# Kernel optimization log

Hardware: AMD Instinct MI355X
Metric: run time of the kernel (lower is better)

Reference implementation:

```python
import jax, jax.numpy as jnp
import numpy as np

TAU = 2.0        # tau_m
EPS = 1e-5       # BatchNorm eps
SG_GAIN = 4.0    # surrogate gradient gain for LIF nodes
GATE_GAIN = 10.0 # SCALPerceptionLayer gain
GATE_VTH = 0.5   # SCALPerceptionLayer v_th_init


def _spike(v, v_th, gain):
    # Heaviside forward, sigmoid surrogate backward (straight-through).
    s = jax.nn.sigmoid(gain * (v - v_th))
    hard = (v >= v_th).astype(v.dtype)
    return s + jax.lax.stop_gradient(hard - s)


def _lif(x, v_th):
    # single-step LIF, zero initial membrane: v = v0 + (x - v0)/tau = x/tau
    return _spike(x / TAU, v_th, SG_GAIN)


def _bn(x, gamma, beta):
    # BatchNorm1d over channel dim D of (B, N, D): stats over (B, N)
    m = x.mean(axis=(0, 1))
    v = x.var(axis=(0, 1))
    return (x - m) * jax.lax.rsqrt(v + EPS) * gamma + beta


def setup_inputs() -> dict:
    B, N, D, H = 4, 1024, 1024, 16
    key = jax.random.key(0)
    ks = jax.random.split(key, 12)
    def lin(k, out_f, in_f):
        return jax.random.normal(k, (out_f, in_f), jnp.float32) * (in_f ** -0.5)
    inp = {"x": jax.random.normal(ks[0], (B, N, D), jnp.float32)}
    for i, nm in enumerate(["q", "k", "v", "p"]):
        inp[f"W{nm}"] = lin(ks[1 + i], D, D)
        inp[f"b{nm}"] = jnp.zeros((D,), jnp.float32)
        inp[f"g{nm}"] = jnp.ones((D,), jnp.float32)   # BN gamma
        inp[f"beta{nm}"] = jnp.zeros((D,), jnp.float32)  # BN beta
    inp["Wg"] = lin(ks[10], H, D)  # logic_core linear
    inp["bg"] = jnp.zeros((H,), jnp.float32)
    return inp


def reference(x, Wq, bq, gq, betaq, Wk, bk, gk, betak,
              Wv, bv, gv, betav, Wp, bp, gp, betap, Wg, bg):
    B, N, D = x.shape
    H = Wg.shape[0]
    hd = D // H
    scale = hd ** -0.125

    def branch(W, b, g, beta):
        # Linear -> BN (over channels) -> LIF spike -> (B,H,N,hd)
        s = _lif(_bn(x @ W.T + b, g, beta), 1.0)
        return s.reshape(B, N, H, hd).transpose(0, 2, 1, 3)

    q = branch(Wq, bq, gq, betaq)
    k = branch(Wk, bk, gk, betak)
    v = branch(Wv, bv, gv, betav)

    # LogicGateController: energy (B,H) -> repeat to (B,D) -> spiking linear gate
    energy = (q * k).sum(axis=-1).mean(axis=-1)            # (B, H)
    energy_feat = jnp.tile(energy, (1, D // H))            # (B, D)
    gate = _spike(energy_feat @ Wg.T + bg, GATE_VTH, GATE_GAIN)  # (B, H)
    gate = gate[:, :, None, None]                          # (B, H, 1, 1)

    attn = jnp.einsum('bhnd,bhmd->bhnm', q, k) * scale     # (B,H,N,N)
    x_attn = jnp.einsum('bhnm,bhmd->bhnd', attn * gate, v) # (B,H,N,hd)
    x_attn = x_attn.transpose(0, 2, 1, 3).reshape(B, N, D)
    x_attn = _lif(x_attn, 0.5)                             # attn_lif, v_th=0.5

    out = _lif(_bn(x_attn @ Wp.T + bp, gp, betap), 1.0)    # proj path
    return out
```

## Files before the change

### kernel.cpp

```cpp
#include <hip/hip_runtime.h>
#include <cstddef>
#include <cstdint>

#define EPS 1e-5f

typedef __bf16 bf16x8 __attribute__((ext_vector_type(8)));
typedef float f32x4 __attribute__((ext_vector_type(4)));
typedef unsigned short u16x8 __attribute__((ext_vector_type(8)));

__device__ __forceinline__ unsigned short f2bf(float f) {
  unsigned u = __builtin_bit_cast(unsigned, f);
  unsigned r = u + 0x7FFFu + ((u >> 16) & 1u);
  return (unsigned short)(r >> 16);
}
__device__ __forceinline__ float bf2f(unsigned short h) {
  unsigned u = (unsigned)h << 16;
  return __builtin_bit_cast(float, u);
}

__device__ __forceinline__ void gl_lds16(const void* g, void* l) {
  __builtin_amdgcn_global_load_lds(
      (const __attribute__((address_space(1))) unsigned int*)g,
      (__attribute__((address_space(3))) unsigned int*)l, 16, 0, 0);
}

template <int MODE>
__global__ __launch_bounds__(512) void gemm8_bf16_bt(
    const unsigned short* __restrict__ A,
    const unsigned short* __restrict__ W0, const unsigned short* __restrict__ W1,
    const float* __restrict__ b0, const float* __restrict__ b1,
    unsigned short* __restrict__ Y, double* __restrict__ psum, double* __restrict__ psq,
    const int* __restrict__ flags, int N, int Kc)
{
  if (MODE == 2) { if (flags[0] == 0) return; }

  __shared__ unsigned short As[2][8192];
  __shared__ unsigned short Bs[2][8192];
  const int tid = threadIdx.x;

  const int bid = blockIdx.x + (blockIdx.y << 3) + (blockIdx.z << 8);
  const int nwg = (int)gridDim.z << 8;
  const int cpx = nwg >> 3;
  const int sw = (bid & 7) * cpx + (bid >> 3);
  const int bx = sw & 7, by = (sw >> 3) & 31, z = sw >> 8;

  if (MODE == 1) { if (flags[1 + (by >> 3)] == 0) return; }

  const unsigned short* Bm = z ? W1 : W0;
  const float* bias = z ? b1 : b0;
  unsigned short* Yz = Y + (size_t)z * 4096 * N;

  const int bm = by * 128, bn = bx * 128;
  const int lane = tid & 63, w = tid >> 6;
  const int wr = w >> 2, wc = w & 3;
  const int l15 = lane & 15, g = lane >> 4;

  f32x4 acc[4][2] = {};

  const unsigned short* aSrc[2]; const unsigned short* bSrc[2]; int dOff[2];
#pragma unroll
  for (int c = 0; c < 2; ++c) {
    int S = c * 512 + tid;
    int row = S >> 3, sp = S & 7;
    int sl = sp ^ (row & 7);
    aSrc[c] = A  + (size_t)(bm + row) * Kc + sl * 8;
    bSrc[c] = Bm + (size_t)(bn + row) * Kc + sl * 8;
    dOff[c] = S * 8;
  }
  int aOff[4][2], bOff[2][2];
#pragma unroll
  for (int t = 0; t < 2; ++t) {
#pragma unroll
    for (int i = 0; i < 4; ++i) {
      int rowA = wr * 64 + i * 16 + l15;
      aOff[i][t] = rowA * 64 + ((t * 4 + g) ^ (rowA & 7)) * 8;
    }
#pragma unroll
    for (int j = 0; j < 2; ++j) {
      int rowB = wc * 32 + j * 16 + l15;
      bOff[j][t] = rowB * 64 + ((t * 4 + g) ^ (rowB & 7)) * 8;
    }
  }

  const int nk = Kc >> 6;
#pragma unroll
  for (int c = 0; c < 2; ++c) { gl_lds16(aSrc[c], &As[0][dOff[c]]); aSrc[c] += 64; }
#pragma unroll
  for (int c = 0; c < 2; ++c) { gl_lds16(bSrc[c], &Bs[0][dOff[c]]); bSrc[c] += 64; }

  int cur = 0;
  for (int kt = 0; kt < nk; ++kt) {
    if (kt + 1 < nk) {
#pragma unroll
      for (int c = 0; c < 2; ++c) { gl_lds16(aSrc[c], &As[cur ^ 1][dOff[c]]); aSrc[c] += 64; }
#pragma unroll
      for (int c = 0; c < 2; ++c) { gl_lds16(bSrc[c], &Bs[cur ^ 1][dOff[c]]); bSrc[c] += 64; }
      asm volatile("s_waitcnt vmcnt(4)" ::: "memory");
    } else {
      asm volatile("s_waitcnt vmcnt(0)" ::: "memory");
    }
    __builtin_amdgcn_s_barrier();
    __builtin_amdgcn_sched_barrier(0);
    {
      const unsigned short* Ac = &As[cur][0];
      const unsigned short* Bc = &Bs[cur][0];
#pragma unroll
      for (int t = 0; t < 2; ++t) {
        bf16x8 af[4], bfr[2];
#pragma unroll
        for (int i = 0; i < 4; ++i) af[i] = *(const bf16x8*)&Ac[aOff[i][t]];
#pragma unroll
        for (int j = 0; j < 2; ++j) bfr[j] = *(const bf16x8*)&Bc[bOff[j][t]];
#pragma unroll
        for (int i = 0; i < 4; ++i)
#pragma unroll
          for (int j = 0; j < 2; ++j)
            acc[i][j] = __builtin_amdgcn_mfma_f32_16x16x32_bf16(af[i], bfr[j], acc[i][j], 0, 0, 0);
      }
    }
    __builtin_amdgcn_s_barrier();
    cur ^= 1;
  }

  const int r0 = bm + wr * 64 + g * 4;
  float csum[2], csq[2];
#pragma unroll
  for (int j = 0; j < 2; ++j) { csum[j] = 0.f; csq[j] = 0.f; }
#pragma unroll
  for (int j = 0; j < 2; ++j) {
    int col = bn + wc * 32 + j * 16 + l15;
    float bv = bias[col];
#pragma unroll
    for (int i = 0; i < 4; ++i)
#pragma unroll
      for (int r = 0; r < 4; ++r) {
        float yv = acc[i][j][r] + bv;
        unsigned short h = f2bf(yv);
        float yb = bf2f(h);
        Yz[(size_t)(r0 + i * 16 + r) * N + col] = h;
        csum[j] += yb;
        csq[j] += yb * yb;
      }
  }
  __syncthreads();
  float* Ls = (float*)&As[0][0];
  const int slot = wr * 4 + g;
#pragma unroll
  for (int j = 0; j < 2; ++j) {
    int ci = wc * 32 + j * 16 + l15;
    Ls[slot * 128 + ci] = csum[j];
    Ls[1024 + slot * 128 + ci] = csq[j];
  }
  __syncthreads();
  if (tid < 128) {
    double s = 0.0, q = 0.0;
#pragma unroll
    for (int sl = 0; sl < 8; ++sl) {
      s += (double)Ls[sl * 128 + tid];
      q += (double)Ls[1024 + sl * 128 + tid];
    }
    size_t o = ((size_t)z * 32 + by) * N + bn + tid;
    psum[o] = s;
    psq[o] = q;
  }
}

__global__ void prep1_kernel(const float* __restrict__ x,
                             const float* __restrict__ Wq, const float* __restrict__ Wk,
                             unsigned short* __restrict__ Xh, unsigned short* __restrict__ Wh3)
{
  int bid = blockIdx.x, tid = threadIdx.x;
  const float* src; unsigned short* dst; size_t base;
  if (bid < 2048) {
    src = x; dst = Xh; base = ((size_t)bid * 256 + tid) * 8;
  } else if (bid < 2560) {
    src = Wq; dst = Wh3; base = ((size_t)(bid - 2048) * 256 + tid) * 8;
  } else {
    src = Wk; dst = Wh3 + (size_t)1024 * 1024; base = ((size_t)(bid - 2560) * 256 + tid) * 8;
  }
  float4 a = *reinterpret_cast<const float4*>(&src[base]);
  float4 b = *reinterpret_cast<const float4*>(&src[base + 4]);
  u16x8 o;
  o[0] = f2bf(a.x); o[1] = f2bf(a.y); o[2] = f2bf(a.z); o[3] = f2bf(a.w);
  o[4] = f2bf(b.x); o[5] = f2bf(b.y); o[6] = f2bf(b.z); o[7] = f2bf(b.w);
  *reinterpret_cast<u16x8*>(&dst[base]) = o;
}

__global__ void prep2_kernel(const float* __restrict__ Wv, const float* __restrict__ Wp,
                             unsigned short* __restrict__ Whv, unsigned short* __restrict__ Wpcat,
                             const int* __restrict__ flags)
{
  if (flags[0] == 0) return;
  int bid = blockIdx.x, tid = threadIdx.x;
  if (bid < 512) {
    size_t base = ((size_t)bid * 256 + tid) * 8;
    float4 a = *reinterpret_cast<const float4*>(&Wv[base]);
    float4 b = *reinterpret_cast<const float4*>(&Wv[base + 4]);
    u16x8 o;
    o[0] = f2bf(a.x); o[1] = f2bf(a.y); o[2] = f2bf(a.z); o[3] = f2bf(a.w);
    o[4] = f2bf(b.x); o[5] = f2bf(b.y); o[6] = f2bf(b.z); o[7] = f2bf(b.w);
    *reinterpret_cast<u16x8*>(&Whv[base]) = o;
  } else {
    size_t base = ((size_t)(bid - 512) * 256 + tid) * 8;
    int r = (int)(base >> 10), c = (int)(base & 1023);
    float4 a = *reinterpret_cast<const float4*>(&Wp[base]);
    float4 b = *reinterpret_cast<const float4*>(&Wp[base + 4]);
    u16x8 hi, lo;
    hi[0] = f2bf(a.x); lo[0] = f2bf(a.x - bf2f(hi[0]));
    hi[1] = f2bf(a.y); lo[1] = f2bf(a.y - bf2f(hi[1]));
    hi[2] = f2bf(a.z); lo[2] = f2bf(a.z - bf2f(hi[2]));
    hi[3] = f2bf(a.w); lo[3] = f2bf(a.w - bf2f(hi[3]));
    hi[4] = f2bf(b.x); lo[4] = f2bf(b.x - bf2f(hi[4]));
    hi[5] = f2bf(b.y); lo[5] = f2bf(b.y - bf2f(hi[5]));
    hi[6] = f2bf(b.z); lo[6] = f2bf(b.z - bf2f(hi[6]));
    hi[7] = f2bf(b.w); lo[7] = f2bf(b.w - bf2f(hi[7]));
    unsigned short* Or = Wpcat + (size_t)r * 2048;
    *reinterpret_cast<u16x8*>(&Or[c]) = hi;
    *reinterpret_cast<u16x8*>(&Or[1024 + c]) = lo;
  }
}

__global__ void bn_finalize(const double* __restrict__ psum, const double* __restrict__ psq,
                            const float* __restrict__ g0, const float* __restrict__ g1,
                            float* __restrict__ meanv, float* __restrict__ Av,
                            const int* __restrict__ runflag,
                            int* __restrict__ zflags, int* __restrict__ zenergy,
                            int N, double invM)
{
  if (zflags && blockIdx.x == 0 && blockIdx.y == 0) {
    int t = threadIdx.x;
    if (t < 5) zflags[t] = 0;
    if (t >= 64 && t < 128) zenergy[t - 64] = 0;
  }
  if (runflag && runflag[0] == 0) return;
  int z = blockIdx.y;
  const float* g = z ? g1 : g0;
  int c = blockIdx.x * blockDim.x + threadIdx.x;
  const double* ps = psum + (size_t)z * 32 * N + c;
  const double* pq = psq  + (size_t)z * 32 * N + c;
  double s0 = 0, s1 = 0, q0 = 0, q1 = 0;
#pragma unroll
  for (int rb = 0; rb < 32; rb += 2) {
    s0 += ps[(size_t)rb * N];       q0 += pq[(size_t)rb * N];
    s1 += ps[(size_t)(rb + 1) * N]; q1 += pq[(size_t)(rb + 1) * N];
  }
  double s = s0 + s1, q = q0 + q1;
  double m = s * invM;
  double var = q * invM - m * m;
  if (var < 0.0) var = 0.0;
  meanv[(size_t)z * N + c] = (float)m;
  Av[(size_t)z * N + c] = g[(size_t)c] * rsqrtf((float)var + EPS);
}

__global__ void bn_finalize_p(const double* __restrict__ psum, const double* __restrict__ psq,
                              const float* __restrict__ gp, const float* __restrict__ bp,
                              float* __restrict__ meanv, float* __restrict__ Av,
                              const int* __restrict__ flags, int N, double invM)
{
  int c = blockIdx.x * blockDim.x + threadIdx.x;
  float ybb = bf2f(f2bf(bp[c]));
  double yd = (double)ybb;
  double s = 0.0, q = 0.0;
  for (int rb = 0; rb < 32; ++rb) {
    if (flags[1 + (rb >> 3)]) {
      s += psum[(size_t)rb * N + c];
      q += psq [(size_t)rb * N + c];
    } else {
      s += 128.0 * yd;
      q += 128.0 * yd * yd;
    }
  }
  double m = s * invM;
  double var = q * invM - m * m;
  if (var < 0.0) var = 0.0;
  meanv[c] = (float)m;
  Av[c] = gp[(size_t)c] * rsqrtf((float)var + EPS);
}

__global__ void energy_cnt(const unsigned short* __restrict__ Yq,
                           const unsigned short* __restrict__ Yk,
                           const float* __restrict__ meanv, const float* __restrict__ Av,
                           const float* __restrict__ beq, const float* __restrict__ bek,
                           int* __restrict__ energy_int, int N)
{
  const int tid = threadIdx.x;
  const int c0 = (tid * 8) & (N - 1);
  const int head = c0 >> 6;
  const int batch = blockIdx.x >> 7;
  const float* mq = meanv;     const float* aq = Av;
  const float* mk = meanv + N; const float* ak = Av + N;
  __shared__ int bins[16];
  if (tid < 16) bins[tid] = 0;
  __syncthreads();
  int cnt = 0;
#pragma unroll
  for (int j = 0; j < 4; ++j) {
    size_t base = (size_t)blockIdx.x * 8192 + j * 2048 + tid * 8;
    u16x8 yq = *reinterpret_cast<const u16x8*>(&Yq[base]);
    u16x8 yk = *reinterpret_cast<const u16x8*>(&Yk[base]);
#pragma unroll
    for (int e = 0; e < 8; ++e) {
      bool sq = (bf2f(yq[e]) - mq[c0 + e]) * aq[c0 + e] + beq[c0 + e] >= 2.0f;
      bool sk = (bf2f(yk[e]) - mk[c0 + e]) * ak[c0 + e] + bek[c0 + e] >= 2.0f;
      cnt += (sq && sk) ? 1 : 0;
    }
  }
  atomicAdd(&bins[head], cnt);
  __syncthreads();
  if (tid < 16) atomicAdd(&energy_int[batch * 16 + tid], bins[tid]);
}

__global__ void spike_qk_write(const unsigned short* __restrict__ Yq,
                               const unsigned short* __restrict__ Yk,
                               const float* __restrict__ meanv, const float* __restrict__ Av,
                               const float* __restrict__ beq, const float* __restrict__ bek,
                               unsigned short* __restrict__ qb, unsigned short* __restrict__ kb,
                               const int* __restrict__ flags, int N)
{
  if (flags[0] == 0) return;
  size_t base = ((size_t)blockIdx.x * 256 + threadIdx.x) * 8;
  int c0 = (int)(base & (size_t)(N - 1));
  const float* mq = meanv;     const float* aq = Av;
  const float* mk = meanv + N; const float* ak = Av + N;
  u16x8 yq = *reinterpret_cast<const u16x8*>(&Yq[base]);
  u16x8 yk = *reinterpret_cast<const u16x8*>(&Yk[base]);
  u16x8 oq, ok;
#pragma unroll
  for (int e = 0; e < 8; ++e) {
    oq[e] = ((bf2f(yq[e]) - mq[c0 + e]) * aq[c0 + e] + beq[c0 + e] >= 2.0f) ? 0x3F80 : 0;
    ok[e] = ((bf2f(yk[e]) - mk[c0 + e]) * ak[c0 + e] + bek[c0 + e] >= 2.0f) ? 0x3F80 : 0;
  }
  *reinterpret_cast<u16x8*>(&qb[base]) = oq;
  *reinterpret_cast<u16x8*>(&kb[base]) = ok;
}

__global__ void spike_v(const unsigned short* __restrict__ Yv,
                        const float* __restrict__ meanv, const float* __restrict__ Av,
                        const float* __restrict__ beta, unsigned short* __restrict__ vb,
                        const int* __restrict__ flags, int N)
{
  if (flags[0] == 0) return;
  size_t base = ((size_t)blockIdx.x * 256 + threadIdx.x) * 8;
  int c0 = (int)(base & (size_t)(N - 1));
  u16x8 y8 = *reinterpret_cast<const u16x8*>(&Yv[base]);
  u16x8 o;
#pragma unroll
  for (int e = 0; e < 8; ++e)
    o[e] = ((bf2f(y8[e]) - meanv[c0 + e]) * Av[c0 + e] + beta[c0 + e] >= 2.0f) ? 0x3F80 : 0;
  *reinterpret_cast<u16x8*>(&vb[base]) = o;
}

__global__ void bn_spike_f32(const unsigned short* __restrict__ Y,
                             const float* __restrict__ meanv, const float* __restrict__ Av,
                             const float* __restrict__ beta, const float* __restrict__ bp,
                             const int* __restrict__ flags, float* __restrict__ S, int N)
{
  size_t base = ((size_t)blockIdx.x * 256 + threadIdx.x) * 8;
  int c0 = (int)(base & (size_t)(N - 1));
  int batch = (int)(base >> 20);
  float y[8];
  if (flags[1 + batch]) {
    u16x8 y8 = *reinterpret_cast<const u16x8*>(&Y[base]);
#pragma unroll
    for (int e = 0; e < 8; ++e) y[e] = bf2f(y8[e]);
  } else {
#pragma unroll
    for (int e = 0; e < 8; ++e) y[e] = bf2f(f2bf(bp[c0 + e]));
  }
  float4 o0, o1;
  o0.x = ((y[0] - meanv[c0 + 0]) * Av[c0 + 0] + beta[c0 + 0] >= 2.0f) ? 1.f : 0.f;
  o0.y = ((y[1] - meanv[c0 + 1]) * Av[c0 + 1] + beta[c0 + 1] >= 2.0f) ? 1.f : 0.f;
  o0.z = ((y[2] - meanv[c0 + 2]) * Av[c0 + 2] + beta[c0 + 2] >= 2.0f) ? 1.f : 0.f;
  o0.w = ((y[3] - meanv[c0 + 3]) * Av[c0 + 3] + beta[c0 + 3] >= 2.0f) ? 1.f : 0.f;
  o1.x = ((y[4] - meanv[c0 + 4]) * Av[c0 + 4] + beta[c0 + 4] >= 2.0f) ? 1.f : 0.f;
  o1.y = ((y[5] - meanv[c0 + 5]) * Av[c0 + 5] + beta[c0 + 5] >= 2.0f) ? 1.f : 0.f;
  o1.z = ((y[6] - meanv[c0 + 6]) * Av[c0 + 6] + beta[c0 + 6] >= 2.0f) ? 1.f : 0.f;
  o1.w = ((y[7] - meanv[c0 + 7]) * Av[c0 + 7] + beta[c0 + 7] >= 2.0f) ? 1.f : 0.f;
  *reinterpret_cast<float4*>(&S[base]) = o0;
  *reinterpret_cast<float4*>(&S[base + 4]) = o1;
}

__global__ void gate_kernel(const int* __restrict__ energy_int, const float* __restrict__ Wg,
                            const float* __restrict__ bg, float* __restrict__ gate,
                            int* __restrict__ flags, int D)
{
  int b = blockIdx.x >> 4, hp = blockIdx.x & 15;
  int tid = threadIdx.x;
  float e[16];
#pragma unroll
  for (int h = 0; h < 16; ++h) e[h] = (float)energy_int[b * 16 + h] * (1.f / 1024.f);
  float s = 0.f;
  for (int j = tid; j < D; j += 256) s = fmaf(e[j & 15], Wg[(size_t)hp * D + j], s);
  __shared__ float red[256];
  red[tid] = s;
  __syncthreads();
  for (int off = 128; off; off >>= 1) {
    if (tid < off) red[tid] += red[tid + off];
    __syncthreads();
  }
  if (tid == 0) {
    int gv = (red[0] + bg[hp] >= 0.5f) ? 1 : 0;
    gate[blockIdx.x] = (float)gv;
    if (gv) { atomicOr(&flags[0], 1); atomicOr(&flags[1 + b], 1); }
  }
}

__global__ __launch_bounds__(256) void attn_kernel(
    const unsigned short* __restrict__ qb, const unsigned short* __restrict__ kb,
    const unsigned short* __restrict__ vb, const float* __restrict__ gate,
    const int* __restrict__ flags, unsigned short* __restrict__ xs,
    int Ntok, int D, float scale)
{
  int bh = blockIdx.x;
  int b = bh >> 4, h = bh & 15;
  if (flags[1 + b] == 0) return;
  int n0 = blockIdx.y * 32;
  int tid = threadIdx.x;
  unsigned short* outbase = xs + (size_t)(b * Ntok + n0) * 2048 + h * 64;

  if (gate[bh] == 0.f) {
    ushort4 zv = {0, 0, 0, 0};
    for (int i = tid; i < 32 * 16; i += 256) {
      int r = i >> 4, c4 = (i & 15) << 2;
      *reinterpret_cast<ushort4*>(&outbase[(size_t)r * 2048 + c4]) = zv;
      *reinterpret_cast<ushort4*>(&outbase[(size_t)r * 2048 + 1024 + c4]) = zv;
    }
    return;
  }

  __shared__ float qs[32][68], ks[32][68], vs[32][68], Ss[32][36];
  const unsigned short* qg = qb + (size_t)b * Ntok * D + h * 64;
  const unsigned short* kg = kb + (size_t)b * Ntok * D + h * 64;
  const unsigned short* vg = vb + (size_t)b * Ntok * D + h * 64;

  {
    int r = tid >> 3, c8 = (tid & 7) * 8;
    u16x8 t = *reinterpret_cast<const u16x8*>(&qg[(size_t)(n0 + r) * D + c8]);
#pragma unroll
    for (int e = 0; e < 8; ++e) qs[r][c8 + e] = bf2f(t[e]);
  }

  float acc[8];
#pragma unroll
  for (int j = 0; j < 8; ++j) acc[j] = 0.f;
  const int nloc = tid >> 3;
  const int dd0 = (tid & 7) * 8;

  for (int mt = 0; mt < Ntok / 32; ++mt) {
    int m0 = mt * 32;
    __syncthreads();
    {
      int r = tid >> 3, c8 = (tid & 7) * 8;
      u16x8 tk = *reinterpret_cast<const u16x8*>(&kg[(size_t)(m0 + r) * D + c8]);
      u16x8 tv = *reinterpret_cast<const u16x8*>(&vg[(size_t)(m0 + r) * D + c8]);
#pragma unroll
      for (int e = 0; e < 8; ++e) { ks[r][c8 + e] = bf2f(tk[e]); vs[r][c8 + e] = bf2f(tv[e]); }
    }
    __syncthreads();
    {
      int np = tid >> 3;
      int mp0 = (tid & 7) * 4;
      float s0 = 0.f, s1 = 0.f, s2 = 0.f, s3 = 0.f;
#pragma unroll 8
      for (int d = 0; d < 64; ++d) {
        float qv = qs[np][d];
        s0 = fmaf(qv, ks[mp0 + 0][d], s0);
        s1 = fmaf(qv, ks[mp0 + 1][d], s1);
        s2 = fmaf(qv, ks[mp0 + 2][d], s2);
        s3 = fmaf(qv, ks[mp0 + 3][d], s3);
      }
      Ss[np][mp0 + 0] = s0; Ss[np][mp0 + 1] = s1;
      Ss[np][mp0 + 2] = s2; Ss[np][mp0 + 3] = s3;
    }
    __syncthreads();
#pragma unroll 8
    for (int mp = 0; mp < 32; ++mp) {
      float sv = Ss[nloc][mp];
#pragma unroll
      for (int j = 0; j < 8; ++j) acc[j] = fmaf(sv, vs[mp][dd0 + j], acc[j]);
    }
  }

#pragma unroll
  for (int j = 0; j < 8; ++j) {
    float x = scale * acc[j];
    unsigned short sp = (x >= 1.0f) ? 0x3F80 : 0;
    outbase[(size_t)nloc * 2048 + dd0 + j] = sp;
    outbase[(size_t)nloc * 2048 + 1024 + dd0 + j] = sp;
  }
}

extern "C" void kernel_launch(void* const* d_in, const int* in_sizes, int n_in,
                              void* d_out, int out_size, void* d_ws, size_t ws_size,
                              hipStream_t stream)
{
  (void)in_sizes; (void)n_in; (void)out_size; (void)ws_size;
  const int Ntok = 1024, D = 1024;
  const int M = 4096;
  const float scale = 0.5946035575013605f;

  const float* x     = (const float*)d_in[0];
  const float* Wq    = (const float*)d_in[1];
  const float* bq    = (const float*)d_in[2];
  const float* gq    = (const float*)d_in[3];
  const float* betaq = (const float*)d_in[4];
  const float* Wk    = (const float*)d_in[5];
  const float* bk    = (const float*)d_in[6];
  const float* gk    = (const float*)d_in[7];
  const float* betak = (const float*)d_in[8];
  const float* Wv    = (const float*)d_in[9];
  const float* bv    = (const float*)d_in[10];
  const float* gv    = (const float*)d_in[11];
  const float* betav = (const float*)d_in[12];
  const float* Wp    = (const float*)d_in[13];
  const float* bp    = (const float*)d_in[14];
  const float* gp    = (const float*)d_in[15];
  const float* betap = (const float*)d_in[16];
  const float* Wg    = (const float*)d_in[17];
  const float* bg    = (const float*)d_in[18];

  char* w = (char*)d_ws;
  const size_t MB = 1024 * 1024;
  const size_t MN = (size_t)M * D;
  unsigned short* Y3bf  = (unsigned short*)(w + 0 * MB);
  unsigned short* xat2  = (unsigned short*)(w + 0 * MB);
  unsigned short* Yv    = Y3bf + 2 * MN;
  unsigned short* Yp    = (unsigned short*)(w + 24 * MB);
  unsigned short* Wpcat = (unsigned short*)(w + 32 * MB);
  unsigned short* Xh    = (unsigned short*)(w + 48 * MB);
  unsigned short* Wh3   = (unsigned short*)(w + 56 * MB);
  unsigned short* qb2   = (unsigned short*)(w + 62 * MB);
  unsigned short* kb2   = (unsigned short*)(w + 70 * MB);
  unsigned short* vb2   = (unsigned short*)(w + 78 * MB);
  double* psum   = (double*)(w + 86 * MB);
  double* psq    = (double*)(w + 87 * MB);
  float*  meanv  = (float*)(w + 88 * MB);
  float*  Av     = (float*)(w + 88 * MB + 16384);
  int*    energy_int = (int*)(w + 88 * MB + 32768);
  int*    flags  = (int*)(w + 88 * MB + 32768 + 512);
  float*  gate   = (float*)(w + 88 * MB + 32768 + 1024);

  float* out = (float*)d_out;
  unsigned short* Whq = Wh3;
  unsigned short* Whk = Wh3 + MN / 4;
  unsigned short* Whv = Wh3 + MN / 2;
  float* meanp = meanv + 3 * D;
  float* Avp   = Av + 3 * D;

  prep1_kernel<<<dim3(3072), 256, 0, stream>>>(x, Wq, Wk, Xh, Wh3);

  gemm8_bf16_bt<0><<<dim3(8, 32, 2), 512, 0, stream>>>(
      Xh, Whq, Whk, bq, bk, Y3bf, psum, psq, nullptr, D, 1024);
  bn_finalize<<<dim3(4, 2), 256, 0, stream>>>(
      psum, psq, gq, gk, meanv, Av, nullptr, flags, energy_int, D, 1.0 / M);

  energy_cnt<<<dim3(512), 256, 0, stream>>>(
      Y3bf, Y3bf + MN, meanv, Av, betaq, betak, energy_int, D);
  gate_kernel<<<dim3(64), 256, 0, stream>>>(energy_int, Wg, bg, gate, flags, D);

  spike_qk_write<<<dim3(2048), 256, 0, stream>>>(
      Y3bf, Y3bf + MN, meanv, Av, betaq, betak, qb2, kb2, flags, D);
  prep2_kernel<<<dim3(1024), 256, 0, stream>>>(Wv, Wp, Whv, Wpcat, flags);
  gemm8_bf16_bt<2><<<dim3(8, 32, 1), 512, 0, stream>>>(
      Xh, Whv, Whv, bv, bv, Yv, psum + 2 * 32 * (size_t)D, psq + 2 * 32 * (size_t)D,
      flags, D, 1024);
  bn_finalize<<<dim3(4, 1), 256, 0, stream>>>(
      psum + 2 * 32 * (size_t)D, psq + 2 * 32 * (size_t)D, gv, gv,
      meanv + 2 * D, Av + 2 * D, flags, nullptr, nullptr, D, 1.0 / M);
  spike_v<<<dim3(2048), 256, 0, stream>>>(Yv, meanv + 2 * D, Av + 2 * D, betav, vb2, flags, D);

  attn_kernel<<<dim3(64, Ntok / 32), 256, 0, stream>>>(
      qb2, kb2, vb2, gate, flags, xat2, Ntok, D, scale);

  gemm8_bf16_bt<1><<<dim3(8, 32, 1), 512, 0, stream>>>(
      xat2, Wpcat, Wpcat, bp, bp, Yp, psum, psq, flags, D, 2048);
  bn_finalize_p<<<dim3(4), 256, 0, stream>>>(psum, psq, gp, bp, meanp, Avp, flags, D, 1.0 / M);
  bn_spike_f32<<<dim3(2048), 256, 0, stream>>>(Yp, meanp, Avp, betap, bp, flags, out, D);
}
```

Before: 84.79 us.

## Use 256-thread GEMM with 4x4 MFMA tiles per wave and fused QK output

```diff
diff --git a/kernel.cpp b/kernel.cpp
--- a/kernel.cpp
+++ b/kernel.cpp
@@ -24,10 +24,9 @@
       (__attribute__((address_space(3))) unsigned int*)l, 16, 0, 0);
 }
 
-template <int MODE>
-__global__ __launch_bounds__(512) void gemm8_bf16_bt(
-    const unsigned short* __restrict__ A,
-    const unsigned short* __restrict__ W0, const unsigned short* __restrict__ W1,
+template <int MODE, int NX>
+__global__ __launch_bounds__(256) void gemm4_bf16_bt(
+    const unsigned short* __restrict__ A, const unsigned short* __restrict__ Bmat,
     const float* __restrict__ b0, const float* __restrict__ b1,
     unsigned short* __restrict__ Y, double* __restrict__ psum, double* __restrict__ psq,
     const int* __restrict__ flags, int N, int Kc)
@@ -38,64 +37,56 @@
   __shared__ unsigned short Bs[2][8192];
   const int tid = threadIdx.x;
 
-  const int bid = blockIdx.x + (blockIdx.y << 3) + (blockIdx.z << 8);
-  const int nwg = (int)gridDim.z << 8;
-  const int cpx = nwg >> 3;
+  constexpr int NXL = (NX == 16) ? 4 : 3;
+  const int bid = blockIdx.x + (blockIdx.y << NXL);
+  const int cpx = (NX * 32) >> 3;
   const int sw = (bid & 7) * cpx + (bid >> 3);
-  const int bx = sw & 7, by = (sw >> 3) & 31, z = sw >> 8;
+  const int bx = sw & (NX - 1), by = sw >> NXL;
 
   if (MODE == 1) { if (flags[1 + (by >> 3)] == 0) return; }
-
-  const unsigned short* Bm = z ? W1 : W0;
-  const float* bias = z ? b1 : b0;
-  unsigned short* Yz = Y + (size_t)z * 4096 * N;
 
   const int bm = by * 128, bn = bx * 128;
   const int lane = tid & 63, w = tid >> 6;
-  const int wr = w >> 2, wc = w & 3;
+  const int wr = w >> 1, wc = w & 1;
   const int l15 = lane & 15, g = lane >> 4;
 
-  f32x4 acc[4][2] = {};
-
-  const unsigned short* aSrc[2]; const unsigned short* bSrc[2]; int dOff[2];
-#pragma unroll
-  for (int c = 0; c < 2; ++c) {
-    int S = c * 512 + tid;
+  f32x4 acc[4][4] = {};
+
+  const unsigned short* aSrc[4]; const unsigned short* bSrc[4]; int dOff[4];
+#pragma unroll
+  for (int c = 0; c < 4; ++c) {
+    int S = c * 256 + tid;
     int row = S >> 3, sp = S & 7;
     int sl = sp ^ (row & 7);
-    aSrc[c] = A  + (size_t)(bm + row) * Kc + sl * 8;
-    bSrc[c] = Bm + (size_t)(bn + row) * Kc + sl * 8;
+    aSrc[c] = A    + (size_t)(bm + row) * Kc + sl * 8;
+    bSrc[c] = Bmat + (size_t)(bn + row) * Kc + sl * 8;
     dOff[c] = S * 8;
   }
-  int aOff[4][2], bOff[2][2];
-#pragma unroll
-  for (int t = 0; t < 2; ++t) {
-#pragma unroll
-    for (int i = 0; i < 4; ++i) {
+  int aOff[4][2], bOff[4][2];
+#pragma unroll
+  for (int i = 0; i < 4; ++i)
+#pragma unroll
+    for (int t = 0; t < 2; ++t) {
       int rowA = wr * 64 + i * 16 + l15;
       aOff[i][t] = rowA * 64 + ((t * 4 + g) ^ (rowA & 7)) * 8;
-    }
-#pragma unroll
-    for (int j = 0; j < 2; ++j) {
-      int rowB = wc * 32 + j * 16 + l15;
-      bOff[j][t] = rowB * 64 + ((t * 4 + g) ^ (rowB & 7)) * 8;
-    }
-  }
+      int rowB = wc * 64 + i * 16 + l15;
+      bOff[i][t] = rowB * 64 + ((t * 4 + g) ^ (rowB & 7)) * 8;
+    }
 
   const int nk = Kc >> 6;
 #pragma unroll
-  for (int c = 0; c < 2; ++c) { gl_lds16(aSrc[c], &As[0][dOff[c]]); aSrc[c] += 64; }
-#pragma unroll
-  for (int c = 0; c < 2; ++c) { gl_lds16(bSrc[c], &Bs[0][dOff[c]]); bSrc[c] += 64; }
+  for (int c = 0; c < 4; ++c) { gl_lds16(aSrc[c], &As[0][dOff[c]]); aSrc[c] += 64; }
+#pragma unroll
+  for (int c = 0; c < 4; ++c) { gl_lds16(bSrc[c], &Bs[0][dOff[c]]); bSrc[c] += 64; }
 
   int cur = 0;
   for (int kt = 0; kt < nk; ++kt) {
     if (kt + 1 < nk) {
 #pragma unroll
-      for (int c = 0; c < 2; ++c) { gl_lds16(aSrc[c], &As[cur ^ 1][dOff[c]]); aSrc[c] += 64; }
-#pragma unroll
-      for (int c = 0; c < 2; ++c) { gl_lds16(bSrc[c], &Bs[cur ^ 1][dOff[c]]); bSrc[c] += 64; }
-      asm volatile("s_waitcnt vmcnt(4)" ::: "memory");
+      for (int c = 0; c < 4; ++c) { gl_lds16(aSrc[c], &As[cur ^ 1][dOff[c]]); aSrc[c] += 64; }
+#pragma unroll
+      for (int c = 0; c < 4; ++c) { gl_lds16(bSrc[c], &Bs[cur ^ 1][dOff[c]]); bSrc[c] += 64; }
+      asm volatile("s_waitcnt vmcnt(8)" ::: "memory");
     } else {
       asm volatile("s_waitcnt vmcnt(0)" ::: "memory");
     }
@@ -106,15 +97,15 @@
       const unsigned short* Bc = &Bs[cur][0];
 #pragma unroll
       for (int t = 0; t < 2; ++t) {
-        bf16x8 af[4], bfr[2];
+        bf16x8 af[4], bfr[4];
 #pragma unroll
         for (int i = 0; i < 4; ++i) af[i] = *(const bf16x8*)&Ac[aOff[i][t]];
 #pragma unroll
-        for (int j = 0; j < 2; ++j) bfr[j] = *(const bf16x8*)&Bc[bOff[j][t]];
+        for (int j = 0; j < 4; ++j) bfr[j] = *(const bf16x8*)&Bc[bOff[j][t]];
 #pragma unroll
         for (int i = 0; i < 4; ++i)
 #pragma unroll
-          for (int j = 0; j < 2; ++j)
+          for (int j = 0; j < 4; ++j)
             acc[i][j] = __builtin_amdgcn_mfma_f32_16x16x32_bf16(af[i], bfr[j], acc[i][j], 0, 0, 0);
       }
     }
@@ -123,13 +114,13 @@
   }
 
   const int r0 = bm + wr * 64 + g * 4;
-  float csum[2], csq[2];
-#pragma unroll
-  for (int j = 0; j < 2; ++j) { csum[j] = 0.f; csq[j] = 0.f; }
-#pragma unroll
-  for (int j = 0; j < 2; ++j) {
-    int col = bn + wc * 32 + j * 16 + l15;
-    float bv = bias[col];
+  float csum[4], csq[4];
+#pragma unroll
+  for (int j = 0; j < 4; ++j) { csum[j] = 0.f; csq[j] = 0.f; }
+#pragma unroll
+  for (int j = 0; j < 4; ++j) {
+    int col = bn + wc * 64 + j * 16 + l15;
+    float bv = (MODE == 0) ? ((col >> 10) ? b1[col & 1023] : b0[col]) : b0[col];
 #pragma unroll
     for (int i = 0; i < 4; ++i)
 #pragma unroll
@@ -137,7 +128,7 @@
         float yv = acc[i][j][r] + bv;
         unsigned short h = f2bf(yv);
         float yb = bf2f(h);
-        Yz[(size_t)(r0 + i * 16 + r) * N + col] = h;
+        Y[(size_t)(r0 + i * 16 + r) * N + col] = h;
         csum[j] += yb;
         csq[j] += yb * yb;
       }
@@ -146,8 +137,8 @@
   float* Ls = (float*)&As[0][0];
   const int slot = wr * 4 + g;
 #pragma unroll
-  for (int j = 0; j < 2; ++j) {
-    int ci = wc * 32 + j * 16 + l15;
+  for (int j = 0; j < 4; ++j) {
+    int ci = wc * 64 + j * 16 + l15;
     Ls[slot * 128 + ci] = csum[j];
     Ls[1024 + slot * 128 + ci] = csq[j];
   }
@@ -159,7 +150,7 @@
       s += (double)Ls[sl * 128 + tid];
       q += (double)Ls[1024 + sl * 128 + tid];
     }
-    size_t o = ((size_t)z * 32 + by) * N + bn + tid;
+    size_t o = (size_t)by * N + bn + tid;
     psum[o] = s;
     psq[o] = q;
   }
@@ -220,42 +211,62 @@
   }
 }
 
-__global__ void bn_finalize(const double* __restrict__ psum, const double* __restrict__ psq,
-                            const float* __restrict__ g0, const float* __restrict__ g1,
-                            float* __restrict__ meanv, float* __restrict__ Av,
-                            const int* __restrict__ runflag,
-                            int* __restrict__ zflags, int* __restrict__ zenergy,
-                            int N, double invM)
-{
-  if (zflags && blockIdx.x == 0 && blockIdx.y == 0) {
+__global__ void bn_finalize_qk(const double* __restrict__ psum, const double* __restrict__ psq,
+                               const float* __restrict__ gq, const float* __restrict__ gk,
+                               float* __restrict__ meanv, float* __restrict__ Av,
+                               int* __restrict__ zflags, int* __restrict__ zenergy,
+                               double invM)
+{
+  if (blockIdx.x == 0) {
     int t = threadIdx.x;
     if (t < 5) zflags[t] = 0;
     if (t >= 64 && t < 128) zenergy[t - 64] = 0;
   }
-  if (runflag && runflag[0] == 0) return;
-  int z = blockIdx.y;
-  const float* g = z ? g1 : g0;
   int c = blockIdx.x * blockDim.x + threadIdx.x;
-  const double* ps = psum + (size_t)z * 32 * N + c;
-  const double* pq = psq  + (size_t)z * 32 * N + c;
+  const double* ps = psum + c;
+  const double* pq = psq + c;
   double s0 = 0, s1 = 0, q0 = 0, q1 = 0;
 #pragma unroll
   for (int rb = 0; rb < 32; rb += 2) {
-    s0 += ps[(size_t)rb * N];       q0 += pq[(size_t)rb * N];
-    s1 += ps[(size_t)(rb + 1) * N]; q1 += pq[(size_t)(rb + 1) * N];
+    s0 += ps[(size_t)rb * 2048];       q0 += pq[(size_t)rb * 2048];
+    s1 += ps[(size_t)(rb + 1) * 2048]; q1 += pq[(size_t)(rb + 1) * 2048];
   }
   double s = s0 + s1, q = q0 + q1;
   double m = s * invM;
   double var = q * invM - m * m;
   if (var < 0.0) var = 0.0;
-  meanv[(size_t)z * N + c] = (float)m;
-  Av[(size_t)z * N + c] = g[(size_t)c] * rsqrtf((float)var + EPS);
+  float gv = (c >> 10) ? gk[c & 1023] : gq[c];
+  meanv[c] = (float)m;
+  Av[c] = gv * rsqrtf((float)var + EPS);
+}
+
+__global__ void bn_finalize_v(const double* __restrict__ psum, const double* __restrict__ psq,
+                              const float* __restrict__ gv,
+                              float* __restrict__ meanv, float* __restrict__ Av,
+                              const int* __restrict__ runflag, double invM)
+{
+  if (runflag[0] == 0) return;
+  int c = blockIdx.x * blockDim.x + threadIdx.x;
+  const double* ps = psum + c;
+  const double* pq = psq + c;
+  double s0 = 0, s1 = 0, q0 = 0, q1 = 0;
+#pragma unroll
+  for (int rb = 0; rb < 32; rb += 2) {
+    s0 += ps[(size_t)rb * 1024];       q0 += pq[(size_t)rb * 1024];
+    s1 += ps[(size_t)(rb + 1) * 1024]; q1 += pq[(size_t)(rb + 1) * 1024];
+  }
+  double s = s0 + s1, q = q0 + q1;
+  double m = s * invM;
+  double var = q * invM - m * m;
+  if (var < 0.0) var = 0.0;
+  meanv[c] = (float)m;
+  Av[c] = gv[(size_t)c] * rsqrtf((float)var + EPS);
 }
 
 __global__ void bn_finalize_p(const double* __restrict__ psum, const double* __restrict__ psq,
                               const float* __restrict__ gp, const float* __restrict__ bp,
                               float* __restrict__ meanv, float* __restrict__ Av,
-                              const int* __restrict__ flags, int N, double invM)
+                              const int* __restrict__ flags, double invM)
 {
   int c = blockIdx.x * blockDim.x + threadIdx.x;
   float ybb = bf2f(f2bf(bp[c]));
@@ -263,8 +274,8 @@
   double s = 0.0, q = 0.0;
   for (int rb = 0; rb < 32; ++rb) {
     if (flags[1 + (rb >> 3)]) {
-      s += psum[(size_t)rb * N + c];
-      q += psq [(size_t)rb * N + c];
+      s += psum[(size_t)rb * 1024 + c];
+      q += psq [(size_t)rb * 1024 + c];
     } else {
       s += 128.0 * yd;
       q += 128.0 * yd * yd;
@@ -277,27 +288,30 @@
   Av[c] = gp[(size_t)c] * rsqrtf((float)var + EPS);
 }
 
-__global__ void energy_cnt(const unsigned short* __restrict__ Yq,
-                           const unsigned short* __restrict__ Yk,
+__global__ void energy_cnt(const unsigned short* __restrict__ Yqk,
                            const float* __restrict__ meanv, const float* __restrict__ Av,
                            const float* __restrict__ beq, const float* __restrict__ bek,
-                           int* __restrict__ energy_int, int N)
+                           int* __restrict__ energy_int)
 {
   const int tid = threadIdx.x;
-  const int c0 = (tid * 8) & (N - 1);
+  const int half = tid >> 7;
+  const int tloc = tid & 127;
+  const int c0 = tloc * 8;
   const int head = c0 >> 6;
+  const int r0 = blockIdx.x * 8;
   const int batch = blockIdx.x >> 7;
-  const float* mq = meanv;     const float* aq = Av;
-  const float* mk = meanv + N; const float* ak = Av + N;
+  const float* mq = meanv;        const float* aq = Av;
+  const float* mk = meanv + 1024; const float* ak = Av + 1024;
   __shared__ int bins[16];
   if (tid < 16) bins[tid] = 0;
   __syncthreads();
   int cnt = 0;
 #pragma unroll
   for (int j = 0; j < 4; ++j) {
-    size_t base = (size_t)blockIdx.x * 8192 + j * 2048 + tid * 8;
-    u16x8 yq = *reinterpret_cast<const u16x8*>(&Yq[base]);
-    u16x8 yk = *reinterpret_cast<const u16x8*>(&Yk[base]);
+    int row = r0 + j * 2 + half;
+    size_t base = (size_t)row * 2048 + c0;
+    u16x8 yq = *reinterpret_cast<const u16x8*>(&Yqk[base]);
+    u16x8 yk = *reinterpret_cast<const u16x8*>(&Yqk[base + 1024]);
 #pragma unroll
     for (int e = 0; e < 8; ++e) {
       bool sq = (bf2f(yq[e]) - mq[c0 + e]) * aq[c0 + e] + beq[c0 + e] >= 2.0f;
@@ -310,28 +324,29 @@
   if (tid < 16) atomicAdd(&energy_int[batch * 16 + tid], bins[tid]);
 }
 
-__global__ void spike_qk_write(const unsigned short* __restrict__ Yq,
-                               const unsigned short* __restrict__ Yk,
+__global__ void spike_qk_write(const unsigned short* __restrict__ Yqk,
                                const float* __restrict__ meanv, const float* __restrict__ Av,
                                const float* __restrict__ beq, const float* __restrict__ bek,
                                unsigned short* __restrict__ qb, unsigned short* __restrict__ kb,
-                               const int* __restrict__ flags, int N)
+                               const int* __restrict__ flags)
 {
   if (flags[0] == 0) return;
-  size_t base = ((size_t)blockIdx.x * 256 + threadIdx.x) * 8;
-  int c0 = (int)(base & (size_t)(N - 1));
-  const float* mq = meanv;     const float* aq = Av;
-  const float* mk = meanv + N; const float* ak = Av + N;
-  u16x8 yq = *reinterpret_cast<const u16x8*>(&Yq[base]);
-  u16x8 yk = *reinterpret_cast<const u16x8*>(&Yk[base]);
+  int idx = blockIdx.x * 256 + threadIdx.x;
+  int r = idx >> 7, c0 = (idx & 127) * 8;
+  const float* mq = meanv;        const float* aq = Av;
+  const float* mk = meanv + 1024; const float* ak = Av + 1024;
+  size_t src = (size_t)r * 2048 + c0;
+  u16x8 yq = *reinterpret_cast<const u16x8*>(&Yqk[src]);
+  u16x8 yk = *reinterpret_cast<const u16x8*>(&Yqk[src + 1024]);
   u16x8 oq, ok;
 #pragma unroll
   for (int e = 0; e < 8; ++e) {
     oq[e] = ((bf2f(yq[e]) - mq[c0 + e]) * aq[c0 + e] + beq[c0 + e] >= 2.0f) ? 0x3F80 : 0;
     ok[e] = ((bf2f(yk[e]) - mk[c0 + e]) * ak[c0 + e] + bek[c0 + e] >= 2.0f) ? 0x3F80 : 0;
   }
-  *reinterpret_cast<u16x8*>(&qb[base]) = oq;
-  *reinterpret_cast<u16x8*>(&kb[base]) = ok;
+  size_t dst = (size_t)r * 1024 + c0;
+  *reinterpret_cast<u16x8*>(&qb[dst]) = oq;
+  *reinterpret_cast<u16x8*>(&kb[dst]) = ok;
 }
 
 __global__ void spike_v(const unsigned short* __restrict__ Yv,
@@ -522,9 +537,9 @@
   char* w = (char*)d_ws;
   const size_t MB = 1024 * 1024;
   const size_t MN = (size_t)M * D;
-  unsigned short* Y3bf  = (unsigned short*)(w + 0 * MB);
+  unsigned short* Yqk   = (unsigned short*)(w + 0 * MB);
   unsigned short* xat2  = (unsigned short*)(w + 0 * MB);
-  unsigned short* Yv    = Y3bf + 2 * MN;
+  unsigned short* Yv    = (unsigned short*)(w + 16 * MB);
   unsigned short* Yp    = (unsigned short*)(w + 24 * MB);
   unsigned short* Wpcat = (unsigned short*)(w + 32 * MB);
   unsigned short* Xh    = (unsigned short*)(w + 48 * MB);
@@ -532,8 +547,10 @@
   unsigned short* qb2   = (unsigned short*)(w + 62 * MB);
   unsigned short* kb2   = (unsigned short*)(w + 70 * MB);
   unsigned short* vb2   = (unsigned short*)(w + 78 * MB);
-  double* psum   = (double*)(w + 86 * MB);
-  double* psq    = (double*)(w + 87 * MB);
+  double* psum_qk = (double*)(w + 86 * MB);
+  double* psq_qk  = (double*)(w + 86 * MB + 524288);
+  double* psum_v  = (double*)(w + 87 * MB);
+  double* psq_v   = (double*)(w + 87 * MB + 262144);
   float*  meanv  = (float*)(w + 88 * MB);
   float*  Av     = (float*)(w + 88 * MB + 16384);
   int*    energy_int = (int*)(w + 88 * MB + 32768);
@@ -541,39 +558,34 @@
   float*  gate   = (float*)(w + 88 * MB + 32768 + 1024);
 
   float* out = (float*)d_out;
-  unsigned short* Whq = Wh3;
-  unsigned short* Whk = Wh3 + MN / 4;
-  unsigned short* Whv = Wh3 + MN / 2;
-  float* meanp = meanv + 3 * D;
-  float* Avp   = Av + 3 * D;
+  unsigned short* Whqk = Wh3;
+  unsigned short* Whv  = Wh3 + 2 * (size_t)D * D;
+  float* meanvv = meanv + 2 * D;  float* Avv = Av + 2 * D;
+  float* meanp  = meanv + 3 * D;  float* Avp = Av + 3 * D;
 
   prep1_kernel<<<dim3(3072), 256, 0, stream>>>(x, Wq, Wk, Xh, Wh3);
 
-  gemm8_bf16_bt<0><<<dim3(8, 32, 2), 512, 0, stream>>>(
-      Xh, Whq, Whk, bq, bk, Y3bf, psum, psq, nullptr, D, 1024);
-  bn_finalize<<<dim3(4, 2), 256, 0, stream>>>(
-      psum, psq, gq, gk, meanv, Av, nullptr, flags, energy_int, D, 1.0 / M);
-
-  energy_cnt<<<dim3(512), 256, 0, stream>>>(
-      Y3bf, Y3bf + MN, meanv, Av, betaq, betak, energy_int, D);
+  gemm4_bf16_bt<0, 16><<<dim3(16, 32, 1), 256, 0, stream>>>(
+      Xh, Whqk, bq, bk, Yqk, psum_qk, psq_qk, nullptr, 2048, 1024);
+  bn_finalize_qk<<<dim3(8), 256, 0, stream>>>(
+      psum_qk, psq_qk, gq, gk, meanv, Av, flags, energy_int, 1.0 / M);
+
+  energy_cnt<<<dim3(512), 256, 0, stream>>>(Yqk, meanv, Av, betaq, betak, energy_int);
   gate_kernel<<<dim3(64), 256, 0, stream>>>(energy_int, Wg, bg, gate, flags, D);
 
   spike_qk_write<<<dim3(2048), 256, 0, stream>>>(
-      Y3bf, Y3bf + MN, meanv, Av, betaq, betak, qb2, kb2, flags, D);
+      Yqk, meanv, Av, betaq, betak, qb2, kb2, flags);
   prep2_kernel<<<dim3(1024), 256, 0, stream>>>(Wv, Wp, Whv, Wpcat, flags);
-  gemm8_bf16_bt<2><<<dim3(8, 32, 1), 512, 0, stream>>>(
-      Xh, Whv, Whv, bv, bv, Yv, psum + 2 * 32 * (size_t)D, psq + 2 * 32 * (size_t)D,
-      flags, D, 1024);
-  bn_finalize<<<dim3(4, 1), 256, 0, stream>>>(
-      psum + 2 * 32 * (size_t)D, psq + 2 * 32 * (size_t)D, gv, gv,
-      meanv + 2 * D, Av + 2 * D, flags, nullptr, nullptr, D, 1.0 / M);
-  spike_v<<<dim3(2048), 256, 0, stream>>>(Yv, meanv + 2 * D, Av + 2 * D, betav, vb2, flags, D);
+  gemm4_bf16_bt<2, 8><<<dim3(8, 32, 1), 256, 0, stream>>>(
+      Xh, Whv, bv, bv, Yv, psum_v, psq_v, flags, 1024, 1024);
+  bn_finalize_v<<<dim3(4), 256, 0, stream>>>(psum_v, psq_v, gv, meanvv, Avv, flags, 1.0 / M);
+  spike_v<<<dim3(2048), 256, 0, stream>>>(Yv, meanvv, Avv, betav, vb2, flags, D);
 
   attn_kernel<<<dim3(64, Ntok / 32), 256, 0, stream>>>(
       qb2, kb2, vb2, gate, flags, xat2, Ntok, D, scale);
 
-  gemm8_bf16_bt<1><<<dim3(8, 32, 1), 512, 0, stream>>>(
-      xat2, Wpcat, Wpcat, bp, bp, Yp, psum, psq, flags, D, 2048);
-  bn_finalize_p<<<dim3(4), 256, 0, stream>>>(psum, psq, gp, bp, meanp, Avp, flags, D, 1.0 / M);
+  gemm4_bf16_bt<1, 8><<<dim3(8, 32, 1), 256, 0, stream>>>(
+      xat2, Wpcat, bp, bp, Yp, psum_qk, psq_qk, flags, 1024, 2048);
+  bn_finalize_p<<<dim3(4), 256, 0, stream>>>(psum_qk, psq_qk, gp, bp, meanp, Avp, flags, 1.0 / M);
   bn_spike_f32<<<dim3(2048), 256, 0, stream>>>(Yp, meanp, Avp, betap, bp, flags, out, D);
 }
```

Measured after the change: 85.23 us. No clear change (+0.5%).
